# Kernel tuning notes

Hardware: AMD Instinct MI355X
Metric: run time of the kernel (lower is better)

## Reference

```python
import jax, jax.numpy as jnp
import numpy as np

B, S, V, D = 32, 512, 256, 512          # batch, seq, vocab, embedding_dim
NSYM, NCON = 512, 64                     # VQ codebook sizes
DEPTH, LOOK, MEMSPAN = 6, 3, 10          # recursion depth, lookahead, memory span
CC = 0.25                                # commitment cost
EPS = 1e-8


def setup_inputs() -> dict:
    key = jax.random.key(0)
    ks = jax.random.split(key, 16)
    n = jax.random.normal
    s = 1.0 / np.sqrt(D)
    s2 = 1.0 / np.sqrt(2 * D)
    return {
        "x": jax.random.randint(ks[0], (B, S), 0, V),
        "mag": n(ks[1], (V, D), jnp.float32),
        "phase": n(ks[2], (V, D), jnp.float32),
        "Wr": n(ks[3], (D, D), jnp.float32) * s,      # ComplexLinear real weight
        "Wi": n(ks[4], (D, D), jnp.float32) * s,      # ComplexLinear imag weight
        "qw": n(ks[5], (D, 2 * D), jnp.float32) * s2,  # attention Q: Linear(2d -> d)
        "qb": jnp.zeros((D,), jnp.float32),
        "kw": n(ks[6], (D, 2 * D), jnp.float32) * s2,
        "kb": jnp.zeros((D,), jnp.float32),
        "vw": n(ks[7], (2 * D, 2 * D), jnp.float32) * s2,  # V: Linear(2d -> 2d)
        "vb": jnp.zeros((2 * D,), jnp.float32),
        "dec_w": n(ks[8], (V, 2 * D), jnp.float32) * s2,
        "dec_b": jnp.zeros((V,), jnp.float32),
        "sym": n(ks[9], (NSYM, 2 * D), jnp.float32),
        "con": n(ks[10], (NCON, 2 * D), jnp.float32),
    }


def reference(x, mag, phase, Wr, Wi, qw, qb, kw, kb, vw, vb, dec_w, dec_b, sym, con):
    sg = jax.lax.stop_gradient
    scale = D ** (-0.5)

    def cell(zr, zi):
        # complex linear: (Wr + i Wi)(zr + i zi)
        lr = zr @ Wr.T - zi @ Wi.T
        li = zi @ Wr.T + zr @ Wi.T
        m = jnp.sqrt(lr * lr + li * li + EPS)
        lr = lr / (1.0 + m)
        li = li / (1.0 + m)
        return jnp.tanh(lr), jnp.tanh(li)

    def attend(mem, zr, zi, conf):
        # history: list of (zr, zi); stacked along new axis 2 -> [B,S,M,2D]
        Q = jnp.concatenate([zr, zi], -1) @ qw.T + qb           # [B,S,D]
        H = jnp.stack([jnp.concatenate([mr, mi], -1) for mr, mi in mem], 2)
        K = H @ kw.T + kb                                        # [B,S,M,D]
        Vv = H @ vw.T + vb                                       # [B,S,M,2D]
        scores = jnp.einsum('bsd,bsmd->bsm', Q, K) * scale
        if conf is not None:
            scores = scores * conf[..., None]
        w = jax.nn.softmax(scores, axis=-1)
        ctx = jnp.einsum('bsm,bsme->bse', w, Vv)                 # [B,S,2D]
        return zr + 0.1 * ctx[..., :D], zi + 0.1 * ctx[..., D:]

    def quantize(z, book):
        # squared euclidean distances to codebook rows
        d = (z * z).sum(-1, keepdims=True) + (book * book).sum(-1) - 2.0 * z @ book.T
        idx = jnp.argmin(d, -1)                                  # [B,S]
        dist = jnp.min(d, -1)
        zq = book[idx]
        loss = jnp.mean((zq - sg(z)) ** 2) + CC * jnp.mean((sg(zq) - z) ** 2)
        zq = z + sg(zq - z)  # straight-through
        return zq, loss, idx, dist

    # embed: magnitude * e^{i phase}
    r = mag[x]
    t = phase[x]
    zr, zi = r * jnp.cos(t), r * jnp.sin(t)

    mem = []
    conf = None
    symL = jnp.float32(0.0)
    conL = jnp.float32(0.0)
    for _ in range(DEPTH):
        zr, zi = cell(zr, zi)
        if mem:
            zr, zi = attend(mem, zr, zi, conf)
        zf = jnp.concatenate([zr, zi], -1)
        zs, ls, si, sd = quantize(zf, sym)
        zc, lc, ci, _ = quantize(zs, con)
        zr, zi = zs[..., :D], zs[..., D:]
        symL = symL + ls
        conL = conL + lc
        conf = 1.0 / (1.0 + sd)
        mem.append((zr, zi))
        mem = mem[-MEMSPAN:]

    for _ in range(LOOK):
        zr, zi = cell(zr, zi)

    out = jnp.concatenate([zr, zi], -1) @ dec_w.T + dec_b        # [B,S,V]
    return out, symL, conL
```

## Files before the change

### kernel.cpp

```cpp
#include <hip/hip_runtime.h>
#include <math.h>

constexpr int DD    = 512;
constexpr int D2    = 1024;
constexpr int NTOK  = 256;
constexpr int NSYM  = 512;
constexpr int NCON  = 64;
constexpr int VOCAB = 256;
constexpr int BS_TOT = 32 * 512;
constexpr int NDEPTH = 6;
constexpr int NLOOK  = 3;
constexpr float EPSF = 1e-8f;
constexpr float SCALE = 0.044194173824159216f;

__device__ inline void fma4(float4& a, const float4& w, float s) {
    a.x += w.x * s; a.y += w.y * s; a.z += w.z * s; a.w += w.w * s;
}

__device__ inline float wave_sum(float x) {
#pragma unroll
    for (int off = 32; off; off >>= 1) x += __shfl_xor(x, off, 64);
    return x;
}

__device__ inline void wave_argmin(float& d, int& i) {
#pragma unroll
    for (int off = 32; off; off >>= 1) {
        float od = __shfl_xor(d, off, 64);
        int   oi = __shfl_xor(i, off, 64);
        if (od < d || (od == d && oi < i)) { d = od; i = oi; }
    }
}

__device__ __forceinline__ void d_gemmT(const float* __restrict__ WT,
                                        const float* __restrict__ X,
                                        float* __restrict__ P, int N,
                                        int j0, int t0, int k0, int NC, int slot,
                                        int mstr,
                                        float* __restrict__ sX, float* __restrict__ sW) {
    constexpr int LDT = 68;
    int tid = threadIdx.x;
    int jq = tid & 15;
    int tq = tid >> 4;
    int f0 = tid * 2, f1 = tid * 2 + 1;
    int tA0 = f0 >> 3, kqA0 = f0 & 7;
    int tA1 = f1 >> 3, kqA1 = f1 & 7;
    int kwB0 = f0 >> 4, jB0 = f0 & 15;
    int kwB1 = f1 >> 4, jB1 = f1 & 15;
    float4 vx0, vx1, vw0, vw1;

#define GLOAD(kbase) do { \
        vx0 = *(const float4*)&X[(size_t)(t0 + tA0) * D2 + (kbase) + kqA0 * 4]; \
        vx1 = *(const float4*)&X[(size_t)(t0 + tA1) * D2 + (kbase) + kqA1 * 4]; \
        vw0 = *(const float4*)&WT[(size_t)((kbase) + kwB0) * N + j0 + jB0 * 4]; \
        vw1 = *(const float4*)&WT[(size_t)((kbase) + kwB1) * N + j0 + jB1 * 4]; \
    } while (0)
#define LSTORE(bufi) do { \
        float* sxB = sX + (bufi) * 2176; float* swB = sW + (bufi) * 2176; \
        sxB[(kqA0 * 4 + 0) * LDT + tA0] = vx0.x; \
        sxB[(kqA0 * 4 + 1) * LDT + tA0] = vx0.y; \
        sxB[(kqA0 * 4 + 2) * LDT + tA0] = vx0.z; \
        sxB[(kqA0 * 4 + 3) * LDT + tA0] = vx0.w; \
        sxB[(kqA1 * 4 + 0) * LDT + tA1] = vx1.x; \
        sxB[(kqA1 * 4 + 1) * LDT + tA1] = vx1.y; \
        sxB[(kqA1 * 4 + 2) * LDT + tA1] = vx1.z; \
        sxB[(kqA1 * 4 + 3) * LDT + tA1] = vx1.w; \
        *(float4*)&swB[kwB0 * LDT + jB0 * 4] = vw0; \
        *(float4*)&swB[kwB1 * LDT + jB1 * 4] = vw1; \
    } while (0)

    float4 acc0 = {0,0,0,0}, acc1 = {0,0,0,0}, acc2 = {0,0,0,0}, acc3 = {0,0,0,0};

    GLOAD(k0);
    LSTORE(0);
    __syncthreads();

    for (int kc = 0; kc < NC; ++kc) {
        if (kc + 1 < NC) GLOAD(k0 + (kc + 1) * 32);
        const float* sxB = sX + (kc & 1) * 2176;
        const float* swB = sW + (kc & 1) * 2176;
#pragma unroll 8
        for (int k = 0; k < 32; ++k) {
            float4 xa = *(const float4*)&sxB[k * LDT + tq * 4];
            float4 wb = *(const float4*)&swB[k * LDT + jq * 4];
            fma4(acc0, wb, xa.x);
            fma4(acc1, wb, xa.y);
            fma4(acc2, wb, xa.z);
            fma4(acc3, wb, xa.w);
        }
        if (kc + 1 < NC) LSTORE((kc + 1) & 1);
        __syncthreads();
    }
#undef GLOAD
#undef LSTORE

    size_t base = ((size_t)slot * mstr + (t0 + tq * 4)) * N + j0 + jq * 4;
    *(float4*)&P[base]         = acc0;
    *(float4*)&P[base + N]     = acc1;
    *(float4*)&P[base + 2*N]   = acc2;
    *(float4*)&P[base + 3*N]   = acc3;
}

template<int KB>
__global__ __launch_bounds__(256) void gemmT_kernel(const float* __restrict__ WT,
                                                    const float* __restrict__ X,
                                                    float* __restrict__ P,
                                                    int N) {
    __shared__ __align__(16) float sX[2 * 2176];
    __shared__ __align__(16) float sW[2 * 2176];
    d_gemmT(WT, X, P, N, blockIdx.x * 64, blockIdx.y * 64,
            blockIdx.z * KB, KB / 32, blockIdx.z, NTOK, sX, sW);
}

__global__ __launch_bounds__(256) void precomp2_kernel(const float* __restrict__ CW,
                                                       const float* __restrict__ KVT,
                                                       const float* __restrict__ sym,
                                                       float* __restrict__ SCP,
                                                       float* __restrict__ SKVP) {
    __shared__ __align__(16) float sX[2 * 2176];
    __shared__ __align__(16) float sW[2 * 2176];
    int b = blockIdx.x;
    if (b < 512) {
        int s = b & 3, tile = b >> 2;
        int jx = tile & 15, tx = tile >> 4;
        d_gemmT(CW, sym, SCP, 1024, jx * 64, tx * 64, s * 256, 8, s, NSYM, sX, sW);
    } else {
        int q = b - 512;
        int s = q & 1, tile = q >> 1;
        int jx = tile % 24, tx = tile / 24;
        d_gemmT(KVT, sym, SKVP, 1536, jx * 64, tx * 64, s * 512, 16, s, NSYM, sX, sW);
    }
}

__global__ __launch_bounds__(256) void precombine_kernel(const float* __restrict__ SCP,
                                                         const float* __restrict__ SKVP,
                                                         float* __restrict__ SC,
                                                         float* __restrict__ SKV) {
    int b = blockIdx.x, tid = threadIdx.x;
    if (b < 512) {
        int c = b;
#pragma unroll
        for (int r = 0; r < 4; ++r) {
            int j = r * 256 + tid;
            float v = 0.f;
#pragma unroll
            for (int s = 0; s < 4; ++s)
                v += SCP[((size_t)s * NSYM + c) * 1024 + j];
            SC[(size_t)c * 1024 + j] = v;
        }
    } else {
        int c = b - 512;
#pragma unroll
        for (int r = 0; r < 6; ++r) {
            int e = r * 256 + tid;
            float v = SKVP[(size_t)c * 1536 + e]
                    + SKVP[((size_t)NSYM + c) * 1536 + e];
            SKV[(size_t)c * 1536 + e] = v;
        }
    }
}

__global__ __launch_bounds__(256) void epi_kernel(const float* __restrict__ cellP,
                                                  float* __restrict__ z) {
    int bx = blockIdx.x, t = blockIdx.y, tid = threadIdx.x;
    int j = bx * 256 + tid;
    float lr = 0.f, li = 0.f;
#pragma unroll
    for (int s = 0; s < 8; ++s) {
        lr += cellP[((size_t)s * NTOK + t) * D2 + j];
        li += cellP[((size_t)s * NTOK + t) * D2 + DD + j];
    }
    float m = sqrtf(lr * lr + li * li + EPSF);
    float inv = 1.0f / (1.0f + m);
    z[(size_t)t * D2 + j]      = tanhf(lr * inv);
    z[(size_t)t * D2 + DD + j] = tanhf(li * inv);
}

__global__ __launch_bounds__(256) void attend8_kernel(float* __restrict__ z,
                                                      const float* __restrict__ QP,
                                                      const float* __restrict__ qb,
                                                      const float* __restrict__ Kmem,
                                                      const float* __restrict__ Vmem,
                                                      const float* __restrict__ conf,
                                                      int M) {
    int v = blockIdx.x, tid = threadIdx.x;
    int lane = tid & 63, w = tid >> 6;
    __shared__ float s_part[4][5];
    float q0 = 0.f, q1 = 0.f;
#pragma unroll
    for (int s = 0; s < 8; ++s) {
        q0 += QP[((size_t)s * NTOK + v) * DD + tid];
        q1 += QP[((size_t)s * NTOK + v) * DD + 256 + tid];
    }
    q0 += qb[tid];
    q1 += qb[256 + tid];
    float sc[5];
#pragma unroll
    for (int m = 0; m < 5; ++m) {
        if (m < M) {
            const float* K = Kmem + (size_t)m * NTOK * DD + (size_t)v * DD;
            sc[m] = q0 * K[tid] + q1 * K[256 + tid];
        } else sc[m] = 0.f;
    }
#pragma unroll
    for (int m = 0; m < 5; ++m) {
        if (m < M) {
            float x = wave_sum(sc[m]);
            if (lane == 0) s_part[w][m] = x;
        }
    }
    __syncthreads();
    float cf = conf[v];
    float scf[5];
    float mx = -1e30f;
#pragma unroll
    for (int m = 0; m < 5; ++m) {
        if (m < M) {
            float t = (s_part[0][m] + s_part[1][m] + s_part[2][m] + s_part[3][m]) * SCALE * cf;
            scf[m] = t;
            mx = fmaxf(mx, t);
        }
    }
    float sum = 0.f;
#pragma unroll
    for (int m = 0; m < 5; ++m) {
        if (m < M) { scf[m] = expf(scf[m] - mx); sum += scf[m]; }
    }
    float inv = 1.0f / sum;
#pragma unroll
    for (int r = 0; r < 4; ++r) {
        int e = r * 256 + tid;
        float ctx = 0.f;
#pragma unroll
        for (int m = 0; m < 5; ++m)
            if (m < M) ctx += scf[m] * Vmem[(size_t)m * NTOK * D2 + (size_t)v * D2 + e];
        z[(size_t)v * D2 + e] += 0.1f * ctx * inv;
    }
}

__global__ __launch_bounds__(512) void finishG_kernel(const float* __restrict__ z,
                                                      const float* __restrict__ sym,
                                                      const float* __restrict__ snorm,
                                                      const float* __restrict__ con,
                                                      const float* __restrict__ conT,
                                                      const float* __restrict__ symP,
                                                      float* __restrict__ conf,
                                                      float* __restrict__ symErr,
                                                      float* __restrict__ conErr,
                                                      const float* __restrict__ SC,
                                                      const float* __restrict__ SKV,
                                                      float* __restrict__ zmid,
                                                      const float* __restrict__ kb,
                                                      const float* __restrict__ vb,
                                                      float* __restrict__ Kslot,
                                                      float* __restrict__ Vslot,
                                                      int doKV) {
    int t0 = blockIdx.x, tid = threadIdx.x;
    int lane = tid & 63, w = tid >> 6;
    __shared__ __align__(16) float s_z[D2];
    __shared__ float wA[8];
    __shared__ float wB[8]; __shared__ int wiB[8];
    __shared__ float wC[8], wD[8];
    __shared__ float wE[8];
    __shared__ int   s_ci[1];
    __shared__ float s_pd[512], s_pc[512];

    if (tid < 256) ((float4*)s_z)[tid] = ((const float4*)(z + (size_t)t0 * D2))[tid];
    __syncthreads();
    {
        float a = s_z[tid], b = s_z[512 + tid];
        float nrm = wave_sum(a * a + b * b);
        if (lane == 0) wA[w] = nrm;
    }
    __syncthreads();
    float znorm = 0.f;
#pragma unroll
    for (int k = 0; k < 8; ++k) znorm += wA[k];
    {
        float dot = 0.f;
#pragma unroll
        for (int s = 0; s < 8; ++s)
            dot += symP[((size_t)s * NTOK + t0) * NSYM + tid];
        float d = (znorm + snorm[tid]) - 2.f * dot;
        int idx = tid;
        wave_argmin(d, idx);
        if (lane == 0) { wB[w] = d; wiB[w] = idx; }
    }
    __syncthreads();
    float dmin = wB[0]; int si = wiB[0];
#pragma unroll
    for (int k = 1; k < 8; ++k) {
        if (wB[k] < dmin || (wB[k] == dmin && wiB[k] < si)) { dmin = wB[k]; si = wiB[k]; }
    }
    if (tid == 0) conf[t0] = 1.0f / (1.0f + dmin);
    {
        const float* crow = sym + (size_t)si * D2;
        float errp = 0.f, zn2 = 0.f;
#pragma unroll
        for (int r = 0; r < 2; ++r) {
            int e = r * 512 + tid;
            float zf = s_z[e];
            float diff = crow[e] - zf;
            errp += diff * diff;
            float zn = zf + diff;
            zn2 += zn * zn;
            s_z[e] = zn;
        }
        errp = wave_sum(errp);
        zn2  = wave_sum(zn2);
        if (lane == 0) { wC[w] = errp; wD[w] = zn2; }
    }
    __syncthreads();
    if (tid == 0) {
        float s = 0.f;
#pragma unroll
        for (int k = 0; k < 8; ++k) s += wC[k];
        symErr[t0] += s;
    }
    float zsnorm = 0.f;
#pragma unroll
    for (int k = 0; k < 8; ++k) zsnorm += wD[k];
    {
        int c = tid & 63, sl = tid >> 6;
        float pd = 0.f, pc = 0.f;
        int kk0 = sl * 128;
#pragma unroll 4
        for (int k = kk0; k < kk0 + 128; ++k) {
            float wv = conT[(size_t)k * NCON + c];
            pd += wv * s_z[k];
            pc += wv * wv;
        }
        s_pd[tid] = pd; s_pc[tid] = pc;
    }
    __syncthreads();
    if (tid < 64) {
        float dot2 = 0.f, cn2 = 0.f;
#pragma unroll
        for (int i = 0; i < 8; ++i) { dot2 += s_pd[tid + 64 * i]; cn2 += s_pc[tid + 64 * i]; }
        float dc = (zsnorm + cn2) - 2.f * dot2;
        int ic = tid;
        wave_argmin(dc, ic);
        if (tid == 0) s_ci[0] = ic;
    }
    __syncthreads();
    int ci0 = s_ci[0];
    {
        const float* crow = con + (size_t)ci0 * D2;
        float p = 0.f;
#pragma unroll
        for (int r = 0; r < 2; ++r) {
            int e = r * 512 + tid;
            float diff = crow[e] - s_z[e];
            p += diff * diff;
        }
        p = wave_sum(p);
        if (lane == 0) wE[w] = p;
    }
    __syncthreads();
    if (tid == 0) {
        float s = 0.f;
#pragma unroll
        for (int k = 0; k < 8; ++k) s += wE[k];
        conErr[t0] += s;
    }

    {
        const float* scr = SC + (size_t)si * D2;
        int j = tid;
        float lr = scr[j], li = scr[j + DD];
        float m = sqrtf(lr * lr + li * li + EPSF);
        float inv = 1.0f / (1.0f + m);
        zmid[(size_t)t0 * D2 + j]      = tanhf(lr * inv);
        zmid[(size_t)t0 * D2 + DD + j] = tanhf(li * inv);
        if (doKV) {
            const float* skr = SKV + (size_t)si * 1536;
#pragma unroll
            for (int it = 0; it < 3; ++it) {
                int e = it * 512 + tid;
                float v = skr[e];
                if (e < DD) Kslot[(size_t)t0 * DD + e]        = v + kb[e];
                else        Vslot[(size_t)t0 * D2 + (e - DD)] = v + vb[e - DD];
            }
        }
    }
}

__global__ void deccomb_kernel(const float* __restrict__ P, const float* __restrict__ db,
                               float* __restrict__ rows) {
    int t = blockIdx.x, j = threadIdx.x;
    float v = 0.f;
#pragma unroll
    for (int s = 0; s < 16; ++s)
        v += P[((size_t)s * NTOK + t) * VOCAB + j];
    rows[(size_t)t * VOCAB + j] = v + db[j];
}

__global__ __launch_bounds__(256) void scatterloss_kernel(const int* __restrict__ x,
                                                          const float* __restrict__ rows,
                                                          float* __restrict__ out,
                                                          const float* __restrict__ symErr,
                                                          const float* __restrict__ conErr) {
    int tid = threadIdx.x;
    if (blockIdx.x == BS_TOT / 4) {
        __shared__ int h[256];
        __shared__ double rs[256], rc[256];
        h[tid] = 0;
        __syncthreads();
        for (int i = tid; i < BS_TOT; i += 256) atomicAdd(&h[x[i]], 1);
        __syncthreads();
        rs[tid] = (double)h[tid] * (double)symErr[tid];
        rc[tid] = (double)h[tid] * (double)conErr[tid];
        __syncthreads();
        for (int off = 128; off > 0; off >>= 1) {
            if (tid < off) { rs[tid] += rs[tid + off]; rc[tid] += rc[tid + off]; }
            __syncthreads();
        }
        if (tid == 0) {
            const double denom = (double)BS_TOT * (double)D2;
            out[(size_t)BS_TOT * VOCAB]     = (float)(1.25 * rs[0] / denom);
            out[(size_t)BS_TOT * VOCAB + 1] = (float)(1.25 * rc[0] / denom);
        }
        return;
    }
    int pos = blockIdx.x * 4 + (tid >> 6);
    int lane = tid & 63;
    int v = x[pos];
    const float4* r = (const float4*)(rows + (size_t)v * VOCAB);
    ((float4*)(out + (size_t)pos * VOCAB))[lane] = r[lane];
}

__global__ __launch_bounds__(512) void setup_kernel(const float* __restrict__ qw,
                                                    const float* __restrict__ kw,
                                                    const float* __restrict__ vw,
                                                    const float* __restrict__ sym,
                                                    const float* __restrict__ dec_w,
                                                    const float* __restrict__ con,
                                                    const float* __restrict__ Wr,
                                                    const float* __restrict__ Wi,
                                                    const float* __restrict__ mag,
                                                    const float* __restrict__ phase,
                                                    float* __restrict__ qwT,
                                                    float* __restrict__ KVT,
                                                    float* __restrict__ symT,
                                                    float* __restrict__ decT,
                                                    float* __restrict__ conT,
                                                    float* __restrict__ CW,
                                                    float* __restrict__ dst,
                                                    float* __restrict__ snorm,
                                                    float* __restrict__ symErr,
                                                    float* __restrict__ conErr) {
    __shared__ float t[32][33];
    __shared__ float tr[32][33], ti[32][33];
    __shared__ float s_w[8];
    int b = blockIdx.x;
    int tid = threadIdx.x;

    if (b < 2880) {
        const float* in; float* outp; int ldo;
        if      (b < 512)  {           in = qw;    outp = qwT;      ldo = DD;    }
        else if (b < 1024) { b -= 512; in = kw;    outp = KVT;      ldo = 1536;  }
        else if (b < 2048) { b -= 1024; in = vw;   outp = KVT + DD; ldo = 1536;  }
        else if (b < 2560) { b -= 2048; in = sym;  outp = symT;     ldo = NSYM;  }
        else if (b < 2816) { b -= 2560; in = dec_w; outp = decT;    ldo = VOCAB; }
        else               { b -= 2816; in = con;  outp = conT;     ldo = NCON;  }
        int bx = b & 31, by = b >> 5;
        int c0 = bx * 32, r0 = by * 32;
        int xx = tid & 31, yy = tid >> 5;
#pragma unroll
        for (int i = 0; i < 32; i += 16)
            t[yy + i][xx] = in[(size_t)(r0 + yy + i) * D2 + c0 + xx];
        __syncthreads();
#pragma unroll
        for (int i = 0; i < 32; i += 16)
            outp[(size_t)(c0 + yy + i) * ldo + r0 + xx] = t[xx][yy + i];
        return;
    }
    if (b == 2880) {
        if (tid < 256) { symErr[tid] = 0.f; conErr[tid] = 0.f; }
        return;
    }
    if (b < 3137) {
        int q = b - 2881;
        int j0 = (q & 15) * 32, k0 = (q >> 4) * 32;
        int xx = tid & 31, yy = tid >> 5;
#pragma unroll
        for (int i = 0; i < 32; i += 16) {
            tr[yy + i][xx] = Wr[(size_t)(j0 + yy + i) * DD + k0 + xx];
            ti[yy + i][xx] = Wi[(size_t)(j0 + yy + i) * DD + k0 + xx];
        }
        __syncthreads();
#pragma unroll
        for (int i = 0; i < 32; i += 16) {
            float vr = tr[xx][yy + i];
            float vi = ti[xx][yy + i];
            int k = k0 + yy + i, j = j0 + xx;
            CW[(size_t)k * D2 + j]             = vr;
            CW[(size_t)k * D2 + DD + j]        = vi;
            CW[(size_t)(DD + k) * D2 + j]      = -vi;
            CW[(size_t)(DD + k) * D2 + DD + j] = vr;
        }
        return;
    }
    if (b < 3393) {
        int v = b - 3137, j = tid;
        float r = mag[v * DD + j], th = phase[v * DD + j];
        dst[(size_t)v * D2 + j]      = r * cosf(th);
        dst[(size_t)v * D2 + DD + j] = r * sinf(th);
        return;
    }
    {
        int c = b - 3393;
        float2 vv = ((const float2*)(sym + (size_t)c * D2))[tid];
        float p = vv.x * vv.x + vv.y * vv.y;
        p = wave_sum(p);
        int lane = tid & 63, w = tid >> 6;
        if (lane == 0) s_w[w] = p;
        __syncthreads();
        if (tid == 0) {
            float s = 0.f;
#pragma unroll
            for (int k = 0; k < 8; ++k) s += s_w[k];
            snorm[c] = s;
        }
    }
}

extern "C" void kernel_launch(void* const* d_in, const int* in_sizes, int n_in,
                              void* d_out, int out_size, void* d_ws, size_t ws_size,
                              hipStream_t stream) {
    const int*   x     = (const int*)  d_in[0];
    const float* mag   = (const float*)d_in[1];
    const float* phase = (const float*)d_in[2];
    const float* Wr    = (const float*)d_in[3];
    const float* Wi    = (const float*)d_in[4];
    const float* qw    = (const float*)d_in[5];
    const float* qb    = (const float*)d_in[6];
    const float* kw    = (const float*)d_in[7];
    const float* kb    = (const float*)d_in[8];
    const float* vw    = (const float*)d_in[9];
    const float* vb    = (const float*)d_in[10];
    const float* dec_w = (const float*)d_in[11];
    const float* dec_b = (const float*)d_in[12];
    const float* sym   = (const float*)d_in[13];
    const float* con   = (const float*)d_in[14];
    float* out = (float*)d_out;

    float* ws     = (float*)d_ws;
    float* bufA   = ws;
    float* bufB   = bufA + NTOK * D2;
    float* Kmem   = bufB + NTOK * D2;
    float* Vmem   = Kmem + NDEPTH * NTOK * DD;
    float* rows   = Vmem + NDEPTH * NTOK * D2;
    float* CW     = rows + NTOK * VOCAB;
    float* qwT    = CW + D2 * D2;
    float* KVT    = qwT + D2 * DD;
    float* symT   = KVT + D2 * 1536;
    float* decT   = symT + D2 * NSYM;
    float* conT   = decT + D2 * VOCAB;
    float* bigP   = conT + D2 * NCON;
    float* SC     = bigP + 8 * NTOK * D2;
    float* SKV    = SC + NSYM * D2;
    float* snorm  = bigP + 8 * NTOK * D2 + 4 * NTOK * 1536;
    float* conf   = snorm + NSYM;
    float* symErr = conf + NTOK;
    float* conErr = symErr + NTOK;

    float* QP   = bigP;
    float* symP = bigP + 1048576;
    float* decP = bigP;

    float* SCP  = bigP;
    float* SKVP = Vmem;

    setup_kernel<<<3905, 512, 0, stream>>>(qw, kw, vw, sym, dec_w, con, Wr, Wi, mag, phase,
                                           qwT, KVT, symT, decT, conT, CW,
                                           bufA, snorm, symErr, conErr);
    precomp2_kernel<<<896, 256, 0, stream>>>(CW, KVT, sym, SCP, SKVP);
    precombine_kernel<<<1024, 256, 0, stream>>>(SCP, SKVP, SC, SKV);

    gemmT_kernel<128><<<dim3(16, 4, 8), 256, 0, stream>>>(CW, bufA, bigP, D2);
    epi_kernel<<<dim3(2, 256), 256, 0, stream>>>(bigP, bufB);
    gemmT_kernel<128><<<dim3(8, 4, 8), 256, 0, stream>>>(symT, bufB, symP, NSYM);
    finishG_kernel<<<NTOK, 512, 0, stream>>>(bufB, sym, snorm, con, conT, symP,
                                             conf, symErr, conErr,
                                             SC, SKV, bufA, kb, vb,
                                             Kmem, Vmem, 1);
    float* cur = bufA;
    float* oth = bufB;

    for (int d = 1; d < NDEPTH; ++d) {
        gemmT_kernel<128><<<dim3(8, 4, 8), 256, 0, stream>>>(qwT, cur, QP, DD);
        attend8_kernel<<<NTOK, 256, 0, stream>>>(cur, QP, qb, Kmem, Vmem, conf, d);
        gemmT_kernel<128><<<dim3(8, 4, 8), 256, 0, stream>>>(symT, cur, symP, NSYM);
        finishG_kernel<<<NTOK, 512, 0, stream>>>(cur, sym, snorm, con, conT, symP,
                                                 conf, symErr, conErr,
                                                 SC, SKV, oth, kb, vb,
                                                 Kmem + (size_t)d * NTOK * DD,
                                                 Vmem + (size_t)d * NTOK * D2,
                                                 d < NDEPTH - 1 ? 1 : 0);
        { float* t = cur; cur = oth; oth = t; }
    }

    for (int l = 1; l < NLOOK; ++l) {
        gemmT_kernel<128><<<dim3(16, 4, 8), 256, 0, stream>>>(CW, cur, bigP, D2);
        epi_kernel<<<dim3(2, 256), 256, 0, stream>>>(bigP, oth);
        { float* t = cur; cur = oth; oth = t; }
    }

    gemmT_kernel<64><<<dim3(4, 4, 16), 256, 0, stream>>>(decT, cur, decP, VOCAB);
    deccomb_kernel<<<256, 256, 0, stream>>>(decP, dec_b, rows);
    scatterloss_kernel<<<BS_TOT / 4 + 1, 256, 0, stream>>>(x, rows, out, symErr, conErr);
}
```

Baseline: 438.5 us.

## Precompute per-codeword cell output and query projection, index by quantized symbol

Because the post-quantize state is always a symbol codeword, the cell nonlinearity is now applied once per codeword in the precombine step, and the query projection of those cell outputs is precomputed per codeword (ZMID·qw) in a kernel fused with the first symbol-distance GEMM. The per-depth query GEMM is removed and the attention kernel looks up the query by the stored symbol index. This drops one GEMM launch per depth at the cost of an extra small precompute GEMM and an index buffer written by the finish kernel.

```diff
diff --git a/kernel.cpp b/kernel.cpp
--- a/kernel.cpp
+++ b/kernel.cpp
@@ -132,21 +132,26 @@
     }
 }
 
-__global__ __launch_bounds__(256) void precombine_kernel(const float* __restrict__ SCP,
-                                                         const float* __restrict__ SKVP,
-                                                         float* __restrict__ SC,
-                                                         float* __restrict__ SKV) {
+__global__ __launch_bounds__(256) void precombine2_kernel(const float* __restrict__ SCP,
+                                                          const float* __restrict__ SKVP,
+                                                          float* __restrict__ ZMID,
+                                                          float* __restrict__ SKV) {
     int b = blockIdx.x, tid = threadIdx.x;
     if (b < 512) {
         int c = b;
 #pragma unroll
-        for (int r = 0; r < 4; ++r) {
+        for (int r = 0; r < 2; ++r) {
             int j = r * 256 + tid;
-            float v = 0.f;
-#pragma unroll
-            for (int s = 0; s < 4; ++s)
-                v += SCP[((size_t)s * NSYM + c) * 1024 + j];
-            SC[(size_t)c * 1024 + j] = v;
+            float lr = 0.f, li = 0.f;
+#pragma unroll
+            for (int s = 0; s < 4; ++s) {
+                lr += SCP[((size_t)s * NSYM + c) * 1024 + j];
+                li += SCP[((size_t)s * NSYM + c) * 1024 + j + DD];
+            }
+            float m = sqrtf(lr * lr + li * li + EPSF);
+            float inv = 1.0f / (1.0f + m);
+            ZMID[(size_t)c * D2 + j]      = tanhf(lr * inv);
+            ZMID[(size_t)c * D2 + j + DD] = tanhf(li * inv);
         }
     } else {
         int c = b - 512;
@@ -160,6 +165,26 @@
     }
 }
 
+__global__ __launch_bounds__(256) void symzq_kernel(const float* __restrict__ symT,
+                                                    const float* __restrict__ X,
+                                                    float* __restrict__ symP,
+                                                    const float* __restrict__ qwT,
+                                                    const float* __restrict__ ZMID,
+                                                    float* __restrict__ ZQP) {
+    __shared__ __align__(16) float sX[2 * 2176];
+    __shared__ __align__(16) float sW[2 * 2176];
+    int b = blockIdx.x;
+    if (b < 256) {
+        int jx = b & 7, tx = (b >> 3) & 3, s = b >> 5;
+        d_gemmT(symT, X, symP, NSYM, jx * 64, tx * 64, s * 128, 4, s, NTOK, sX, sW);
+    } else {
+        int q = b - 256;
+        int s = q & 3, tile = q >> 2;
+        int jx = tile & 7, tx = tile >> 3;
+        d_gemmT(qwT, ZMID, ZQP, DD, jx * 64, tx * 64, s * 256, 8, s, NSYM, sX, sW);
+    }
+}
+
 __global__ __launch_bounds__(256) void epi_kernel(const float* __restrict__ cellP,
                                                   float* __restrict__ z) {
     int bx = blockIdx.x, t = blockIdx.y, tid = threadIdx.x;
@@ -176,21 +201,23 @@
     z[(size_t)t * D2 + DD + j] = tanhf(li * inv);
 }
 
-__global__ __launch_bounds__(256) void attend8_kernel(float* __restrict__ z,
-                                                      const float* __restrict__ QP,
+__global__ __launch_bounds__(256) void attendZ_kernel(float* __restrict__ z,
+                                                      const float* __restrict__ ZQP,
                                                       const float* __restrict__ qb,
                                                       const float* __restrict__ Kmem,
                                                       const float* __restrict__ Vmem,
                                                       const float* __restrict__ conf,
+                                                      const int* __restrict__ si,
                                                       int M) {
     int v = blockIdx.x, tid = threadIdx.x;
     int lane = tid & 63, w = tid >> 6;
     __shared__ float s_part[4][5];
+    int sv = si[v];
     float q0 = 0.f, q1 = 0.f;
 #pragma unroll
-    for (int s = 0; s < 8; ++s) {
-        q0 += QP[((size_t)s * NTOK + v) * DD + tid];
-        q1 += QP[((size_t)s * NTOK + v) * DD + 256 + tid];
+    for (int s = 0; s < 4; ++s) {
+        q0 += ZQP[((size_t)s * NSYM + sv) * DD + tid];
+        q1 += ZQP[((size_t)s * NSYM + sv) * DD + 256 + tid];
     }
     q0 += qb[tid];
     q1 += qb[256 + tid];
@@ -238,23 +265,24 @@
     }
 }
 
-__global__ __launch_bounds__(512) void finishG_kernel(const float* __restrict__ z,
-                                                      const float* __restrict__ sym,
-                                                      const float* __restrict__ snorm,
-                                                      const float* __restrict__ con,
-                                                      const float* __restrict__ conT,
-                                                      const float* __restrict__ symP,
-                                                      float* __restrict__ conf,
-                                                      float* __restrict__ symErr,
-                                                      float* __restrict__ conErr,
-                                                      const float* __restrict__ SC,
-                                                      const float* __restrict__ SKV,
-                                                      float* __restrict__ zmid,
-                                                      const float* __restrict__ kb,
-                                                      const float* __restrict__ vb,
-                                                      float* __restrict__ Kslot,
-                                                      float* __restrict__ Vslot,
-                                                      int doKV) {
+__global__ __launch_bounds__(512) void finishG2_kernel(const float* __restrict__ z,
+                                                       const float* __restrict__ sym,
+                                                       const float* __restrict__ snorm,
+                                                       const float* __restrict__ con,
+                                                       const float* __restrict__ conT,
+                                                       const float* __restrict__ symP,
+                                                       float* __restrict__ conf,
+                                                       float* __restrict__ symErr,
+                                                       float* __restrict__ conErr,
+                                                       const float* __restrict__ ZMID,
+                                                       const float* __restrict__ SKV,
+                                                       float* __restrict__ zmid,
+                                                       const float* __restrict__ kb,
+                                                       const float* __restrict__ vb,
+                                                       float* __restrict__ Kslot,
+                                                       float* __restrict__ Vslot,
+                                                       int* __restrict__ siout,
+                                                       int doKV) {
     int t0 = blockIdx.x, tid = threadIdx.x;
     int lane = tid & 63, w = tid >> 6;
     __shared__ __align__(16) float s_z[D2];
@@ -292,7 +320,7 @@
     for (int k = 1; k < 8; ++k) {
         if (wB[k] < dmin || (wB[k] == dmin && wiB[k] < si)) { dmin = wB[k]; si = wiB[k]; }
     }
-    if (tid == 0) conf[t0] = 1.0f / (1.0f + dmin);
+    if (tid == 0) { conf[t0] = 1.0f / (1.0f + dmin); siout[t0] = si; }
     {
         const float* crow = sym + (size_t)si * D2;
         float errp = 0.f, zn2 = 0.f;
@@ -365,13 +393,9 @@
     }
 
     {
-        const float* scr = SC + (size_t)si * D2;
-        int j = tid;
-        float lr = scr[j], li = scr[j + DD];
-        float m = sqrtf(lr * lr + li * li + EPSF);
-        float inv = 1.0f / (1.0f + m);
-        zmid[(size_t)t0 * D2 + j]      = tanhf(lr * inv);
-        zmid[(size_t)t0 * D2 + DD + j] = tanhf(li * inv);
+        const float* zm = ZMID + (size_t)si * D2;
+        zmid[(size_t)t0 * D2 + tid]       = zm[tid];
+        zmid[(size_t)t0 * D2 + 512 + tid] = zm[512 + tid];
         if (doKV) {
             const float* skr = SKV + (size_t)si * 1536;
 #pragma unroll
@@ -558,16 +582,17 @@
     float* decT   = symT + D2 * NSYM;
     float* conT   = decT + D2 * VOCAB;
     float* bigP   = conT + D2 * NCON;
-    float* SC     = bigP + 8 * NTOK * D2;
-    float* SKV    = SC + NSYM * D2;
+    float* ZMID   = bigP + 8 * NTOK * D2;
+    float* SKV    = ZMID + NSYM * D2;
     float* snorm  = bigP + 8 * NTOK * D2 + 4 * NTOK * 1536;
     float* conf   = snorm + NSYM;
     float* symErr = conf + NTOK;
     float* conErr = symErr + NTOK;
-
-    float* QP   = bigP;
+    int*   si     = (int*)(conErr + NTOK);
+
     float* symP = bigP + 1048576;
     float* decP = bigP;
+    float* ZQP  = bigP;
 
     float* SCP  = bigP;
     float* SKVP = Vmem;
@@ -576,28 +601,27 @@
                                            qwT, KVT, symT, decT, conT, CW,
                                            bufA, snorm, symErr, conErr);
     precomp2_kernel<<<896, 256, 0, stream>>>(CW, KVT, sym, SCP, SKVP);
-    precombine_kernel<<<1024, 256, 0, stream>>>(SCP, SKVP, SC, SKV);
+    precombine2_kernel<<<1024, 256, 0, stream>>>(SCP, SKVP, ZMID, SKV);
 
     gemmT_kernel<128><<<dim3(16, 4, 8), 256, 0, stream>>>(CW, bufA, bigP, D2);
     epi_kernel<<<dim3(2, 256), 256, 0, stream>>>(bigP, bufB);
-    gemmT_kernel<128><<<dim3(8, 4, 8), 256, 0, stream>>>(symT, bufB, symP, NSYM);
-    finishG_kernel<<<NTOK, 512, 0, stream>>>(bufB, sym, snorm, con, conT, symP,
-                                             conf, symErr, conErr,
-                                             SC, SKV, bufA, kb, vb,
-                                             Kmem, Vmem, 1);
+    symzq_kernel<<<512, 256, 0, stream>>>(symT, bufB, symP, qwT, ZMID, ZQP);
+    finishG2_kernel<<<NTOK, 512, 0, stream>>>(bufB, sym, snorm, con, conT, symP,
+                                              conf, symErr, conErr,
+                                              ZMID, SKV, bufA, kb, vb,
+                                              Kmem, Vmem, si, 1);
     float* cur = bufA;
     float* oth = bufB;
 
     for (int d = 1; d < NDEPTH; ++d) {
-        gemmT_kernel<128><<<dim3(8, 4, 8), 256, 0, stream>>>(qwT, cur, QP, DD);
-        attend8_kernel<<<NTOK, 256, 0, stream>>>(cur, QP, qb, Kmem, Vmem, conf, d);
+        attendZ_kernel<<<NTOK, 256, 0, stream>>>(cur, ZQP, qb, Kmem, Vmem, conf, si, d);
         gemmT_kernel<128><<<dim3(8, 4, 8), 256, 0, stream>>>(symT, cur, symP, NSYM);
-        finishG_kernel<<<NTOK, 512, 0, stream>>>(cur, sym, snorm, con, conT, symP,
-                                                 conf, symErr, conErr,
-                                                 SC, SKV, oth, kb, vb,
-                                                 Kmem + (size_t)d * NTOK * DD,
-                                                 Vmem + (size_t)d * NTOK * D2,
-                                                 d < NDEPTH - 1 ? 1 : 0);
+        finishG2_kernel<<<NTOK, 512, 0, stream>>>(cur, sym, snorm, con, conT, symP,
+                                                  conf, symErr, conErr,
+                                                  ZMID, SKV, oth, kb, vb,
+                                                  Kmem + (size_t)d * NTOK * DD,
+                                                  Vmem + (size_t)d * NTOK * D2,
+                                                  si, d < NDEPTH - 1 ? 1 : 0);
         { float* t = cur; cur = oth; oth = t; }
     }
 
```

Result: faster. 406.3 us (-7.3%).
